# Optimization experiments

Hardware: AMD Instinct MI355X
Metric: run time of the kernel (lower is better)

The kernel has to match this reference:

```python
import jax, jax.numpy as jnp
import numpy as np
import math

B, S, H, NH = 8, 512, 1024, 16
DH = H // NH
MAX_REL = 64
LN_EPS = 1e-12


def _relpos_table(length, depth, max_rel=MAX_REL):
    # sinusoidal table over relative-distance vocab, gathered into [L, L, depth]
    vocab = 2 * max_rel + 1
    pos = np.arange(vocab, dtype=np.float32)[:, None]
    div = np.exp(np.arange(0, depth, 2, dtype=np.float32) * (-math.log(10000.0) / depth))
    table = np.zeros((vocab, depth), dtype=np.float32)
    table[:, 0::2] = np.sin(pos * div)
    table[:, 1::2] = np.cos(pos * div)
    r = np.arange(length)
    dist = np.clip(r[None, :] - r[:, None], -max_rel, max_rel) + max_rel  # [L,L], entry (i,j)=j-i
    return jnp.asarray(table[dist])  # [L, L, depth]


def _linear(x, W, b):  # torch layout: W [out, in]
    return jnp.einsum('...i,oi->...o', x, W) + b


def _gather_shift(seq, shift, valid_len):
    # seq [B,S,H]; out[i, j] = seq[i, j+shift[i]] for j < valid_len[i], else 0
    pos = jnp.arange(S)
    idx = jnp.clip(pos[None, :] + shift[:, None], 0, S - 1)  # [B,S]
    g = jnp.take_along_axis(seq, idx[:, :, None], axis=1)
    mask = pos[None, :] < valid_len[:, None]
    return jnp.where(mask[:, :, None], g, jnp.zeros((), seq.dtype))


def _nezha_attention(hs, enc, R, Wq, bq, Wk, bk, Wv, bv):
    def heads(x):  # [B,S,H] -> [B,NH,S,DH]
        return x.reshape(B, S, NH, DH).transpose(0, 2, 1, 3)
    q = heads(_linear(hs, Wq, bq))
    k = heads(_linear(enc, Wk, bk))
    v = heads(_linear(enc, Wv, bv))
    scores = jnp.einsum('bhqd,bhkd->bhqk', q, k)
    scores = scores + jnp.einsum('bhqd,qkd->bhqk', q, R)  # relative-key bias
    scores = scores / math.sqrt(DH)
    probs = jax.nn.softmax(scores, axis=-1)  # dropout: eval mode (identity)
    ctx = jnp.einsum('bhqk,bhkd->bhqd', probs, v)
    ctx = ctx + jnp.einsum('bhqk,qkd->bhqd', probs, R)  # relative-value term
    return ctx.transpose(0, 2, 1, 3).reshape(B, S, H)


def setup_inputs() -> dict:
    key = jax.random.key(0)
    ks = jax.random.split(key, 16)
    w = lambda k, shp: jax.random.normal(k, shp, jnp.float32) * 0.02
    return {
        'sequence_output': jax.random.normal(ks[0], (B, S, H), jnp.float32),
        'doc_len': jax.random.randint(ks[1], (B,), 0, 300, jnp.int32),
        'ques_len': jax.random.randint(ks[2], (B,), 0, 100, jnp.int32),
        'option_len': jax.random.randint(ks[3], (B,), 0, 100, jnp.int32),
        'Wq': w(ks[4], (H, H)), 'bq': jnp.zeros((H,), jnp.float32),
        'Wk': w(ks[5], (H, H)), 'bk': jnp.zeros((H,), jnp.float32),
        'Wv': w(ks[6], (H, H)), 'bv': jnp.zeros((H,), jnp.float32),
        'Wp': w(ks[7], (H, H)), 'bp': jnp.zeros((H,), jnp.float32),
        'Wo': w(ks[8], (H, H)), 'bo': jnp.zeros((H,), jnp.float32),
        'ln_g': jnp.ones((H,), jnp.float32), 'ln_b': jnp.zeros((H,), jnp.float32),
    }


def reference(sequence_output, doc_len, ques_len, option_len,
              Wq, bq, Wk, bk, Wv, bv, Wp, bp, Wo, bo, ln_g, ln_b):
    one = jnp.ones_like(doc_len)
    # seperate_seq (only the two tensors DUMA consumes)
    doc_seq = _gather_shift(sequence_output, one, doc_len)
    ques_opt = _gather_shift(sequence_output, doc_len + 1, ques_len + option_len)

    R = _relpos_table(S, DH)
    doc_enc = _nezha_attention(doc_seq, ques_opt, R, Wq, bq, Wk, bk, Wv, bv)
    qo_enc = _nezha_attention(ques_opt, doc_seq, R, Wq, bq, Wk, bk, Wv, bv)

    pooler = lambda x: jnp.tanh(_linear(x, Wp, bp))
    doc_pooled = pooler(doc_enc)
    qo_pooled = pooler(qo_enc)

    # BertSelfOutput: dense + (dropout=eval) + LayerNorm(residual)
    y = _linear(doc_pooled, Wo, bo) + qo_pooled
    mu = jnp.mean(y, axis=-1, keepdims=True)
    var = jnp.mean(jnp.square(y - mu), axis=-1, keepdims=True)
    y = (y - mu) * jax.lax.rsqrt(var + LN_EPS) * ln_g + ln_b

    return pooler(y)
```

## Files before the change

### kernel.cpp

```cpp
#include <hip/hip_runtime.h>
#include <hip/hip_bf16.h>
#include <cstdint>
#include <cstddef>

using bf16 = __hip_bfloat16;
typedef __attribute__((ext_vector_type(8))) short short8;
typedef __attribute__((ext_vector_type(4))) short short4v;
typedef __attribute__((ext_vector_type(4))) float f32x4;

#define KQLD 2048
#define SCL   0.18033688f
#define EXP2F(x) __builtin_amdgcn_exp2f(x)

__device__ __forceinline__ void gl2lds16(const bf16* g, void* l) {
  __builtin_amdgcn_global_load_lds((const __attribute__((address_space(1))) void*)g,
                                   (__attribute__((address_space(3))) void*)l, 16, 0, 0);
}

template<int ACT, bool OUTBF, bool HASB, int VTM>
__global__ __launch_bounds__(512)
void gemm_big(const bf16* __restrict__ A, const bf16* __restrict__ Bm,
              void* __restrict__ Cv, const float* __restrict__ bias,
              int N, int K, int lda, int ldb, int ldc, bf16* __restrict__ Vt,
              const int* __restrict__ dl, const int* __restrict__ ql,
              const int* __restrict__ ol)
{
  __shared__ __align__(16) short lA[3 * 4096];
  __shared__ __align__(16) short lB[3 * 8192];
  const int tid = threadIdx.x;
  int bx = blockIdx.x, by = blockIdx.y;
  {
    const int nwg = gridDim.x * gridDim.y;
    if ((nwg & 7) == 0) {
      int n = by * gridDim.x + bx;
      n = (n & 7) * (nwg >> 3) + (n >> 3);
      bx = n / gridDim.y;
      by = n % gridDim.y;
    }
  }
  const int m0 = bx * 128;
  const int n0 = by * 256;
  const int w = tid >> 6, lane = tid & 63;
  const int wr = (w >> 2) * 64, wc = (w & 3) * 64;
  const int lr = lane & 15, lg = lane >> 4;
  f32x4 acc[4][4] = {};

  bool live = true;
  if (VTM) {
    const int half = m0 >> 12, bb = (m0 >> 9) & 7, j0 = m0 & 511;
    const int vlen = (half == 0) ? dl[bb] : (ql[bb] + ol[bb]);
    live = (j0 < vlen);
  }

  if (live) {
    const int ra = tid >> 2;
    const int xc = ((tid & 3) ^ ((tid >> 2) & 3)) * 8;
    const int e1 = tid + 512;
    const int rb1 = e1 >> 2;
    const bf16* pa0 = A + (long)(m0 + ra) * lda + xc;
    const bf16* pb0 = Bm + (long)(n0 + ra) * ldb + xc;
    const bf16* pb1 = Bm + (long)(n0 + rb1) * ldb + xc;

    #define GSTG(k0_, ofa_, ofb_) do {                  \
      gl2lds16(pa0 + (k0_), &lA[(ofa_) + tid * 8]);     \
      gl2lds16(pb0 + (k0_), &lB[(ofb_) + tid * 8]);     \
      gl2lds16(pb1 + (k0_), &lB[(ofb_) + e1 * 8]);      \
    } while (0)

    const int nT = K >> 5;
    GSTG(0, 0, 0);
    if (nT > 1) GSTG(32, 4096, 8192);
    if (nT > 2) asm volatile("s_waitcnt vmcnt(3)" ::: "memory");
    else        asm volatile("s_waitcnt vmcnt(0)" ::: "memory");
    __builtin_amdgcn_s_barrier();
    __builtin_amdgcn_sched_barrier(0);

    const int lgx = (lg ^ (lr & 3)) * 8;
    int oa = 0, oa1 = 4096, oa2 = 8192;
    int ob = 0, ob1 = 8192, ob2 = 16384;
    for (int t = 0; t < nT; ++t) {
      if (t + 2 < nT) GSTG((t + 2) * 32, oa2, ob2);
      short8 af[4], bfr[4];
      #pragma unroll
      for (int i = 0; i < 4; ++i) {
        af[i]  = *(const short8*)(&lA[oa + (wr + i * 16 + lr) * 32 + lgx]);
        bfr[i] = *(const short8*)(&lB[ob + (wc + i * 16 + lr) * 32 + lgx]);
      }
      #pragma unroll
      for (int mf = 0; mf < 4; ++mf)
        #pragma unroll
        for (int nf = 0; nf < 4; ++nf)
          acc[mf][nf] = __builtin_amdgcn_mfma_f32_16x16x32_bf16(af[mf], bfr[nf], acc[mf][nf], 0, 0, 0);
      if (t + 1 < nT) {
        if (t + 2 < nT) asm volatile("s_waitcnt vmcnt(3)" ::: "memory");
        else            asm volatile("s_waitcnt vmcnt(0)" ::: "memory");
        __builtin_amdgcn_s_barrier();
        __builtin_amdgcn_sched_barrier(0);
        int tmp = oa; oa = oa1; oa1 = oa2; oa2 = tmp;
        tmp = ob; ob = ob1; ob1 = ob2; ob2 = tmp;
      }
    }
    #undef GSTG
  }

  #pragma unroll
  for (int nf = 0; nf < 4; ++nf) {
    const int col = n0 + wc + nf * 16 + lr;
    if (col >= N) continue;
    const float bv = HASB ? bias[col] : 0.0f;
    if (VTM && col >= 2048) {
      const int hd = col - 2048;
      const int d = hd & 63, hh = hd >> 6;
      #pragma unroll
      for (int mf = 0; mf < 4; ++mf) {
        const int row0 = m0 + wr + mf * 16 + lg * 4;
        const int zz = ((1 - (row0 >> 12)) << 7) | (((row0 >> 9) & 7) << 4) | hh;
        short4v pk;
        #pragma unroll
        for (int j = 0; j < 4; ++j)
          pk[j] = (short)__builtin_bit_cast(unsigned short,
                    __float2bfloat16(acc[mf][nf][j] + bv));
        *(short4v*)(Vt + ((long)(zz * 64 + d)) * 512 + (row0 & 511)) = pk;
      }
    } else {
      #pragma unroll
      for (int mf = 0; mf < 4; ++mf) {
        #pragma unroll
        for (int j = 0; j < 4; ++j) {
          const int row = m0 + wr + mf * 16 + lg * 4 + j;
          float x = acc[mf][nf][j] + bv;
          if (ACT == 1) x = tanhf(x);
          const long off = (long)row * ldc + col;
          if (OUTBF) ((bf16*)Cv)[off] = __float2bfloat16(x);
          else       ((float*)Cv)[off] = x;
        }
      }
    }
  }
}

template<int ACT, bool OUTBF>
__global__ __launch_bounds__(256)
void gemm_64(const bf16* __restrict__ A, const bf16* __restrict__ Bm,
             void* __restrict__ Cv, const float* __restrict__ bias,
             int K, int lda, int ldb, int ldc)
{
  __shared__ __align__(16) short lA[3 * 2048];
  __shared__ __align__(16) short lB[3 * 4096];
  const int tid = threadIdx.x;
  int bx = blockIdx.x, by = blockIdx.y;
  {
    const int nwg = gridDim.x * gridDim.y;
    if ((nwg & 7) == 0) {
      int n = by * gridDim.x + bx;
      n = (n & 7) * (nwg >> 3) + (n >> 3);
      bx = n / gridDim.y;
      by = n % gridDim.y;
    }
  }
  const int m0 = bx * 64;
  const int n0 = by * 128;
  const int w = tid >> 6, lane = tid & 63;
  const int wc = w * 32;
  const int lr = lane & 15, lg = lane >> 4;
  f32x4 acc[4][2] = {};
  const int rA = tid >> 2, cA = (tid & 3) * 8;
  const bf16* pa  = A + (long)(m0 + rA) * lda + cA;
  const bf16* pb0 = Bm + (long)(n0 + rA) * ldb + cA;
  const bf16* pb1 = Bm + (long)(n0 + 64 + rA) * ldb + cA;

  #define GS64(k0_, oa_, ob_) do {                     \
    gl2lds16(pa  + (k0_), &lA[(oa_) + tid * 8]);       \
    gl2lds16(pb0 + (k0_), &lB[(ob_) + tid * 8]);       \
    gl2lds16(pb1 + (k0_), &lB[(ob_) + 2048 + tid * 8]);\
  } while (0)

  const int nT = K >> 5;
  GS64(0, 0, 0);
  if (nT > 1) GS64(32, 2048, 4096);
  if (nT > 2) asm volatile("s_waitcnt vmcnt(3)" ::: "memory");
  else        asm volatile("s_waitcnt vmcnt(0)" ::: "memory");
  __builtin_amdgcn_s_barrier();
  __builtin_amdgcn_sched_barrier(0);

  int oa = 0, oa1 = 2048, oa2 = 4096;
  int ob = 0, ob1 = 4096, ob2 = 8192;
  for (int t = 0; t < nT; ++t) {
    if (t + 2 < nT) GS64((t + 2) * 32, oa2, ob2);
    short8 af[4], bfr[2];
    #pragma unroll
    for (int i = 0; i < 4; ++i)
      af[i] = *(const short8*)(&lA[oa + (i * 16 + lr) * 32 + lg * 8]);
    #pragma unroll
    for (int j = 0; j < 2; ++j)
      bfr[j] = *(const short8*)(&lB[ob + (wc + j * 16 + lr) * 32 + lg * 8]);
    #pragma unroll
    for (int mf = 0; mf < 4; ++mf)
      #pragma unroll
      for (int nf = 0; nf < 2; ++nf)
        acc[mf][nf] = __builtin_amdgcn_mfma_f32_16x16x32_bf16(af[mf], bfr[nf], acc[mf][nf], 0, 0, 0);
    if (t + 1 < nT) {
      if (t + 2 < nT) asm volatile("s_waitcnt vmcnt(3)" ::: "memory");
      else            asm volatile("s_waitcnt vmcnt(0)" ::: "memory");
      __builtin_amdgcn_s_barrier();
      __builtin_amdgcn_sched_barrier(0);
      int tmp = oa; oa = oa1; oa1 = oa2; oa2 = tmp;
      tmp = ob; ob = ob1; ob1 = ob2; ob2 = tmp;
    }
  }
  #undef GS64

  #pragma unroll
  for (int nf = 0; nf < 2; ++nf) {
    const int col = n0 + wc + nf * 16 + lr;
    const float bv = bias[col];
    #pragma unroll
    for (int mf = 0; mf < 4; ++mf) {
      #pragma unroll
      for (int j = 0; j < 4; ++j) {
        const int row = m0 + mf * 16 + lg * 4 + j;
        float x = acc[mf][nf][j] + bv;
        if (ACT == 1) x = tanhf(x);
        const long off = (long)row * ldc + col;
        if (OUTBF) ((bf16*)Cv)[off] = __float2bfloat16(x);
        else       ((float*)Cv)[off] = x;
      }
    }
  }
}

__global__ __launch_bounds__(256)
void k_prep(const float* __restrict__ w0, const float* __restrict__ w1,
            const float* __restrict__ w2, const float* __restrict__ w3,
            const float* __restrict__ w4, bf16* __restrict__ wdst,
            const float* __restrict__ seq, const int* __restrict__ dl,
            const int* __restrict__ ql, const int* __restrict__ ol,
            bf16* __restrict__ X, bf16* __restrict__ tbl, bf16* __restrict__ tbt,
            const float* __restrict__ bq, const float* __restrict__ bk,
            const float* __restrict__ bv, float* __restrict__ biasq)
{
  const int bid = blockIdx.x, tid = threadIdx.x;
  if (bid < 5120) {
    const int bsel = bid >> 10;
    const float* s = bsel == 0 ? w0 : bsel == 1 ? w1 : bsel == 2 ? w2 : bsel == 3 ? w3 : w4;
    const float sc = (bsel == 0) ? SCL : 1.0f;
    const long loc = ((long)(bid & 1023) * 256 + tid) * 4;
    float4 v = *(const float4*)(s + loc);
    short4v pk;
    pk[0] = (short)__builtin_bit_cast(unsigned short, __float2bfloat16(v.x * sc));
    pk[1] = (short)__builtin_bit_cast(unsigned short, __float2bfloat16(v.y * sc));
    pk[2] = (short)__builtin_bit_cast(unsigned short, __float2bfloat16(v.z * sc));
    pk[3] = (short)__builtin_bit_cast(unsigned short, __float2bfloat16(v.w * sc));
    *(short4v*)(wdst + (long)bsel * 1048576 + loc) = pk;
  } else if (bid < 13312) {
    const int row = bid - 5120;
    const int c = tid * 4;
    const int b = (row >> 9) & 7, j = row & 511;
    int vlen, src;
    if (row < 4096) { vlen = dl[b]; src = (j + 1 > 511) ? 511 : j + 1; }
    else {
      vlen = ql[b] + ol[b];
      int s2 = j + dl[b] + 1;
      src = s2 > 511 ? 511 : (s2 < 0 ? 0 : s2);
    }
    float4 v = make_float4(0, 0, 0, 0);
    if (j < vlen) v = *(const float4*)(seq + ((long)b * 512 + src) * 1024 + c);
    short4v pk;
    pk[0] = (short)__builtin_bit_cast(unsigned short, __float2bfloat16(v.x));
    pk[1] = (short)__builtin_bit_cast(unsigned short, __float2bfloat16(v.y));
    pk[2] = (short)__builtin_bit_cast(unsigned short, __float2bfloat16(v.z));
    pk[3] = (short)__builtin_bit_cast(unsigned short, __float2bfloat16(v.w));
    *(short4v*)(X + (long)row * 1024 + c) = pk;
  } else {
    for (int idx = tid; idx < 144 * 64; idx += 256) {
      const int r = idx >> 6, d = idx & 63;
      float v = 0.0f;
      if (r < 129) {
        const float dv = powf(10000.0f, -(float)(d >> 1) / 32.0f);
        const float a = (float)r * dv;
        v = (d & 1) ? cosf(a) : sinf(a);
      }
      tbl[idx] = __float2bfloat16(v);
    }
    for (int idx = tid; idx < 64 * 160; idx += 256) {
      const int d = idx / 160, rr = idx % 160;
      float v = 0.0f;
      if (rr < 129) {
        const float dv = powf(10000.0f, -(float)(d >> 1) / 32.0f);
        const float a = (float)rr * dv;
        v = (d & 1) ? cosf(a) : sinf(a);
      }
      tbt[idx] = __float2bfloat16(v);
    }
    for (int idx = tid; idx < 3072; idx += 256) {
      float v = (idx < 1024) ? bq[idx] * SCL : (idx < 2048) ? bk[idx - 1024] : bv[idx - 2048];
      biasq[idx] = v;
    }
  }
}

__global__ __launch_bounds__(1024, 4)
void k_attn(const bf16* __restrict__ QKV, const bf16* __restrict__ Vt,
            const bf16* __restrict__ tbl, const bf16* __restrict__ tbt,
            bf16* __restrict__ ctx)
{
  __shared__ __align__(16) unsigned short s_kv[16384];
  __shared__ __align__(16) unsigned short s_ptile[16][16 * 72];
  __shared__ __align__(16) unsigned short s_m[16][16 * 132];

  const int tid = threadIdx.x;
  const int wv = tid >> 6, lane = tid & 63;
  const int lr = lane & 15, lg = lane >> 4;
  const int bid = blockIdx.x;
  const int xcd = bid & 7;
  const int idx = bid >> 3;
  const int z = (xcd << 5) | (idx >> 1);
  const int g = idx & 1;
  const int attn = z >> 7, b = (z >> 4) & 7, h = z & 15;
  const int qtok0 = attn * 4096 + b * 512;
  const int ktok0 = (1 - attn) * 4096 + b * 512;
  const int q0 = g * 256 + wv * 16;
  const int q = q0 + lr;

  unsigned short* ptile = s_ptile[wv];
  unsigned short* mrow  = s_m[wv];

  const bf16* Kbase = QKV + (long)ktok0 * KQLD + 1024 + h * 64;
  const bf16* Vbase = Vt + (long)z * (64 * 512);

  const int sl = tid & 511;
  const int rs = sl >> 3, cs = (sl & 7) * 8;
  const int scz = cs ^ ((rs & 7) << 3);
  const bool isV = tid >= 512;

  short8 qf[2];
  #pragma unroll
  for (int hh = 0; hh < 2; ++hh)
    qf[hh] = *(const short8*)(QKV + (long)(qtok0 + q0 + lr) * KQLD + h * 64 + hh * 32 + lg * 8);

  #define STAGE(kvb_, koff_, voff_) do {                                            \
    if (!isV) gl2lds16(Kbase + (long)((kvb_) + rs) * KQLD + scz, &s_kv[(koff_) + sl * 8]); \
    else      gl2lds16(Vbase + (long)rs * 512 + (kvb_) + scz,    &s_kv[(voff_) + sl * 8]); \
  } while (0)

  STAGE(0, 0, 8192);

  #pragma unroll
  for (int rt = 0; rt < 9; ++rt) {
    f32x4 qa = {};
    #pragma unroll
    for (int hh = 0; hh < 2; ++hh) {
      short8 ta = *(const short8*)(tbl + (rt * 16 + lr) * 64 + hh * 32 + lg * 8);
      qa = __builtin_amdgcn_mfma_f32_16x16x32_bf16(ta, qf[hh], qa, 0, 0, 0);
    }
    if (rt < 8 || lg == 0) {
      short4v pk;
      #pragma unroll
      for (int j = 0; j < 4; ++j)
        pk[j] = (short)__builtin_bit_cast(unsigned short, __float2bfloat16(qa[j]));
      *(short4v*)(&mrow[lr * 132 + rt * 16 + lg * 4]) = pk;
    }
  }

  const int hx = (lr >> 2) & 1;
  const int lgx8 = (lg ^ (lr & 3)) * 8;
  const int lrx64 = lr * 64;

  const float bias_lo = __bfloat162float(((const bf16*)mrow)[lr * 132 + 0]);
  const float bias_hi = __bfloat162float(((const bf16*)mrow)[lr * 132 + 128]);

  float l_run = 0.f, b0 = 0.f, b1 = 0.f;
  f32x4 cacc[4] = {};

  __syncthreads();

  #pragma unroll 2
  for (int t = 0; t < 8; ++t) {
    const int kvb = t * 64;
    const int koff = (t & 1) * 4096;
    const int voff = 8192 + koff;
    if (t < 7) { const int nk = ((t + 1) & 1) * 4096; STAGE(kvb + 64, nk, 8192 + nk); }

    f32x4 sc[4] = {};
    __builtin_amdgcn_s_setprio(1);
    #pragma unroll
    for (int hh = 0; hh < 2; ++hh) {
      const int cb = ((hh ^ hx) << 5) + lgx8;
      #pragma unroll
      for (int kb4 = 0; kb4 < 4; ++kb4) {
        short8 ak = *(const short8*)(&s_kv[koff + kb4 * 1024 + lrx64 + cb]);
        sc[kb4] = __builtin_amdgcn_mfma_f32_16x16x32_bf16(ak, qf[hh], sc[kb4], 0, 0, 0);
      }
    }
    __builtin_amdgcn_s_setprio(0);

    const int cls = (kvb + 63 <= q0 - 64) ? 0 : ((kvb >= q0 + 79) ? 2 : 1);

    float pacc[4];
    if (cls == 1) {
      const bool eLo = (kvb <= q0 - 49);
      const bool eHi = (kvb + 63 >= q0 + 64);
      short4v pks[4];
      #pragma unroll
      for (int kb4 = 0; kb4 < 4; ++kb4) {
        short4v pk;
        float ps = 0.f;
        #pragma unroll
        for (int j = 0; j < 4; ++j) {
          int rel = kvb + kb4 * 16 + 4 * lg + j - q;
          int rc = rel < -64 ? -64 : (rel > 64 ? 64 : rel);
          float bias = __bfloat162float(((const bf16*)mrow)[lr * 132 + rc + 64]);
          float p = EXP2F(sc[kb4][j] + bias);
          ps += p;
          if (eLo && rel <= -64) b0 += p;
          if (eHi && rel >= 64)  b1 += p;
          pk[j] = (short)__builtin_bit_cast(unsigned short, __float2bfloat16(p));
        }
        pks[kb4] = pk;
        pacc[kb4] = ps;
        *(short4v*)(&ptile[lr * 72 + kb4 * 16 + 4 * lg]) = pk;
      }
      l_run += (pacc[0] + pacc[1]) + (pacc[2] + pacc[3]);
      #pragma unroll
      for (int kb4 = 0; kb4 < 4; ++kb4)
        #pragma unroll
        for (int j = 0; j < 4; ++j) {
          int rel = kvb + kb4 * 16 + 4 * lg + j - q;
          if (rel > -64 && rel < 64)
            mrow[lr * 132 + rel + 63] = (unsigned short)pks[kb4][j];
        }
    } else {
      const float bc = (cls == 0) ? bias_lo : bias_hi;
      #pragma unroll
      for (int kb4 = 0; kb4 < 4; ++kb4) {
        short4v pk;
        float ps = 0.f;
        #pragma unroll
        for (int j = 0; j < 4; ++j) {
          float p = EXP2F(sc[kb4][j] + bc);
          ps += p;
          pk[j] = (short)__builtin_bit_cast(unsigned short, __float2bfloat16(p));
        }
        pacc[kb4] = ps;
        *(short4v*)(&ptile[lr * 72 + kb4 * 16 + 4 * lg]) = pk;
      }
      const float ts = (pacc[0] + pacc[1]) + (pacc[2] + pacc[3]);
      l_run += ts;
      if (cls == 0) b0 += ts; else b1 += ts;
    }

    __builtin_amdgcn_s_setprio(1);
    #pragma unroll
    for (int c2 = 0; c2 < 2; ++c2) {
      short8 pa = *(const short8*)(&ptile[lr * 72 + c2 * 32 + lg * 8]);
      const int cb = ((c2 ^ hx) << 5) + lgx8;
      #pragma unroll
      for (int nf = 0; nf < 4; ++nf) {
        short8 vb = *(const short8*)(&s_kv[voff + nf * 1024 + lrx64 + cb]);
        cacc[nf] = __builtin_amdgcn_mfma_f32_16x16x32_bf16(pa, vb, cacc[nf], 0, 0, 0);
      }
    }
    __builtin_amdgcn_s_setprio(0);
    __syncthreads();
  }
  #undef STAGE

  l_run += __shfl_xor(l_run, 16); l_run += __shfl_xor(l_run, 32);
  b0 += __shfl_xor(b0, 16); b0 += __shfl_xor(b0, 32);
  b1 += __shfl_xor(b1, 16); b1 += __shfl_xor(b1, 32);
  const float inv = 1.0f / l_run;

  #pragma unroll
  for (int j = 0; j < 4; ++j) {
    float iq = __shfl(inv, 4 * lg + j);
    #pragma unroll
    for (int nf = 0; nf < 4; ++nf) cacc[nf][j] *= iq;
  }
  short8 paf[5];
  #pragma unroll
  for (int c = 0; c < 5; ++c)
    #pragma unroll
    for (int j = 0; j < 8; ++j) {
      int r = c * 32 + 8 * lg + j;
      float v = 0.f;
      if (r == 0) v = b0;
      else if (r == 128) v = b1;
      else if (r < 128) {
        int k = q + r - 64;
        if (k >= 0 && k < 512)
          v = __bfloat162float(((const bf16*)mrow)[lr * 132 + r - 1]);
      }
      bf16 vb = __float2bfloat16(v * inv);
      paf[c][j] = (short)__builtin_bit_cast(unsigned short, vb);
    }
  __builtin_amdgcn_s_setprio(1);
  #pragma unroll
  for (int c = 0; c < 5; ++c)
    #pragma unroll
    for (int nf = 0; nf < 4; ++nf) {
      short8 tb = *(const short8*)(tbt + (nf * 16 + lr) * 160 + c * 32 + lg * 8);
      cacc[nf] = __builtin_amdgcn_mfma_f32_16x16x32_bf16(paf[c], tb, cacc[nf], 0, 0, 0);
    }
  __builtin_amdgcn_s_setprio(0);
  #pragma unroll
  for (int nf = 0; nf < 4; ++nf)
    #pragma unroll
    for (int j = 0; j < 4; ++j) {
      int qq = q0 + 4 * lg + j;
      ctx[(long)(qtok0 + qq) * 1024 + h * 64 + nf * 16 + lr] = __float2bfloat16(cacc[nf][j]);
    }
}

__global__ __launch_bounds__(256) void k_ln(const float* __restrict__ y,
    const bf16* __restrict__ pooled, const float* __restrict__ g,
    const float* __restrict__ be, bf16* __restrict__ o)
{
  const int row = blockIdx.x, tid = threadIdx.x;
  float x[4], s1 = 0.0f, s2 = 0.0f;
  #pragma unroll
  for (int i = 0; i < 4; ++i) {
    const int c = tid + i * 256;
    x[i] = y[(long)row * 1024 + c] + __bfloat162float(pooled[(long)(4096 + row) * 1024 + c]);
    s1 += x[i]; s2 += x[i] * x[i];
  }
  #pragma unroll
  for (int off = 1; off < 64; off <<= 1) { s1 += __shfl_xor(s1, off); s2 += __shfl_xor(s2, off); }
  __shared__ float r1[4], r2[4];
  if ((tid & 63) == 0) { r1[tid >> 6] = s1; r2[tid >> 6] = s2; }
  __syncthreads();
  s1 = r1[0] + r1[1] + r1[2] + r1[3];
  s2 = r2[0] + r2[1] + r2[2] + r2[3];
  const float mu = s1 * (1.0f / 1024.0f);
  const float var = s2 * (1.0f / 1024.0f) - mu * mu;
  const float rs = rsqrtf(var + 1e-12f);
  #pragma unroll
  for (int i = 0; i < 4; ++i) {
    const int c = tid + i * 256;
    o[(long)row * 1024 + c] = __float2bfloat16((x[i] - mu) * rs * g[c] + be[c]);
  }
}

__global__ void k_sent(float* o, float v) { o[0] = v; }

extern "C" void kernel_launch(void* const* d_in, const int* in_sizes, int n_in,
                              void* d_out, int out_size, void* d_ws, size_t ws_size,
                              hipStream_t stream)
{
  (void)in_sizes; (void)n_in; (void)out_size;
  const float* seq = (const float*)d_in[0];
  const int*  dl = (const int*)d_in[1];
  const int*  ql = (const int*)d_in[2];
  const int*  ol = (const int*)d_in[3];
  const float* Wq = (const float*)d_in[4];  const float* bq = (const float*)d_in[5];
  const float* Wk = (const float*)d_in[6];  const float* bk = (const float*)d_in[7];
  const float* Wv = (const float*)d_in[8];  const float* bv = (const float*)d_in[9];
  const float* Wp = (const float*)d_in[10]; const float* bp = (const float*)d_in[11];
  const float* Wo = (const float*)d_in[12]; const float* bo = (const float*)d_in[13];
  const float* lng = (const float*)d_in[14]; const float* lnb = (const float*)d_in[15];
  float* out = (float*)d_out;
  char* ws = (char*)d_ws;

  size_t cur = 0;
  auto alloc = [&](size_t bts) { size_t o = cur; cur += (bts + 255) & ~(size_t)255; return o; };
  const size_t oBIAS = alloc(3072 * sizeof(float));
  const size_t oTBL  = alloc(144 * 64 * 2);
  const size_t oTBT  = alloc(64 * 160 * 2);
  const size_t oWBF  = alloc(5ull * 1048576 * 2);
  const size_t oXBF  = alloc(8192ull * 1024 * 2);
  const size_t oQKV  = alloc(8192ull * KQLD * 2);
  const size_t oQR   = alloc(8192ull * 2176 * 2);
  const size_t oBP   = alloc(256ull * 64 * 512 * 2);
  if (ws_size < cur) {
    k_sent<<<1, 1, 0, stream>>>(out, 1.0e6f + (float)(ws_size >> 20));
    return;
  }

  float* biasq = (float*)(ws + oBIAS);
  bf16* tbl = (bf16*)(ws + oTBL);
  bf16* tbt = (bf16*)(ws + oTBT);
  bf16* wqb = (bf16*)(ws + oWBF);
  bf16* wpb = wqb + 3 * 1048576;
  bf16* wob = wqb + 4 * 1048576;
  bf16* xbf = (bf16*)(ws + oXBF);
  bf16* qkv = (bf16*)(ws + oQKV);
  bf16* bpb = (bf16*)(ws + oBP);
  bf16* ctx = xbf;
  bf16* pooled = (bf16*)(ws + oQR);
  float* ybuf = (float*)(ws + oQR + 8192ull * 1024 * 2);
  bf16* yln = (bf16*)(ws + oBP);

  dim3 blk(256);
  k_prep<<<13313, blk, 0, stream>>>(Wq, Wk, Wv, Wp, Wo, wqb,
                                    seq, dl, ql, ol, xbf, tbl, tbt,
                                    bq, bk, bv, biasq);

  gemm_big<0, true, true, 1><<<dim3(64, 12, 1), dim3(512), 0, stream>>>(xbf, wqb, qkv, biasq, 3072, 1024, 1024, 1024, KQLD, bpb, dl, ql, ol);
  k_attn<<<512, dim3(1024), 0, stream>>>(qkv, bpb, tbl, tbt, ctx);

  gemm_64<1, true><<<dim3(128, 8, 1), blk, 0, stream>>>(ctx, wpb, pooled, bp, 1024, 1024, 1024, 1024);
  gemm_64<0, false><<<dim3(64, 8, 1), blk, 0, stream>>>(pooled, wob, ybuf, bo, 1024, 1024, 1024, 1024);
  k_ln<<<4096, blk, 0, stream>>>(ybuf, pooled, lng, lnb, yln);
  gemm_64<1, false><<<dim3(64, 8, 1), blk, 0, stream>>>(yln, wpb, out, bp, 1024, 1024, 1024, 1024);
}
```

Baseline: 236.7 us.

## Skip zero-padded key tiles in attention using analytic padded-key score

Attention now computes how many 64-key tiles hold valid (non-padded) keys from the sequence lengths, and runs the MMA loop only over those tiles. For padded keys, whose K and V rows are just the projection biases, it computes one shared score from a single padded K row and adds the softmax mass and bias-V contribution analytically, still applying the relative-position bias per key. This removes QK and PV matrix work and K/V staging for padded tiles. In exchange the loop is no longer unrolled, extra per-row bookkeeping is added, and correctness relies on padded rows being exactly bias-only, which holds by construction of the gather.

```diff
diff --git a/kernel.cpp b/kernel.cpp
--- a/kernel.cpp
+++ b/kernel.cpp
@@ -302,6 +302,8 @@
 __global__ __launch_bounds__(1024, 4)
 void k_attn(const bf16* __restrict__ QKV, const bf16* __restrict__ Vt,
             const bf16* __restrict__ tbl, const bf16* __restrict__ tbt,
+            const float* __restrict__ biasq, const int* __restrict__ dl,
+            const int* __restrict__ ql, const int* __restrict__ ol,
             bf16* __restrict__ ctx)
 {
   __shared__ __align__(16) unsigned short s_kv[16384];
@@ -322,6 +324,11 @@
   const int q0 = g * 256 + wv * 16;
   const int q = q0 + lr;
 
+  const int vk = (attn == 0) ? (ql[b] + ol[b]) : dl[b];
+  int nLive = (vk + 63) >> 6;
+  if (nLive < 1) nLive = 1;
+  if (nLive > 8) nLive = 8;
+
   unsigned short* ptile = s_ptile[wv];
   unsigned short* mrow  = s_m[wv];
 
@@ -333,10 +340,12 @@
   const int scz = cs ^ ((rs & 7) << 3);
   const bool isV = tid >= 512;
 
-  short8 qf[2];
-  #pragma unroll
-  for (int hh = 0; hh < 2; ++hh)
+  short8 qf[2], kp[2];
+  #pragma unroll
+  for (int hh = 0; hh < 2; ++hh) {
     qf[hh] = *(const short8*)(QKV + (long)(qtok0 + q0 + lr) * KQLD + h * 64 + hh * 32 + lg * 8);
+    kp[hh] = *(const short8*)(Kbase + (long)511 * KQLD + hh * 32 + lg * 8);
+  }
 
   #define STAGE(kvb_, koff_, voff_) do {                                            \
     if (!isV) gl2lds16(Kbase + (long)((kvb_) + rs) * KQLD + scz, &s_kv[(koff_) + sl * 8]); \
@@ -362,6 +371,16 @@
     }
   }
 
+  float sp = 0.f;
+  #pragma unroll
+  for (int hh = 0; hh < 2; ++hh)
+    #pragma unroll
+    for (int j = 0; j < 8; ++j)
+      sp += __bfloat162float(__builtin_bit_cast(bf16, (unsigned short)qf[hh][j])) *
+            __bfloat162float(__builtin_bit_cast(bf16, (unsigned short)kp[hh][j]));
+  sp += __shfl_xor(sp, 16); sp += __shfl_xor(sp, 32);
+  const float s_pad = sp;
+
   const int hx = (lr >> 2) & 1;
   const int lgx8 = (lg ^ (lr & 3)) * 8;
   const int lrx64 = lr * 64;
@@ -369,17 +388,16 @@
   const float bias_lo = __bfloat162float(((const bf16*)mrow)[lr * 132 + 0]);
   const float bias_hi = __bfloat162float(((const bf16*)mrow)[lr * 132 + 128]);
 
-  float l_run = 0.f, b0 = 0.f, b1 = 0.f;
+  float l_run = 0.f, b0 = 0.f, b1 = 0.f, pad_ps = 0.f;
   f32x4 cacc[4] = {};
 
   __syncthreads();
 
-  #pragma unroll 2
-  for (int t = 0; t < 8; ++t) {
+  for (int t = 0; t < nLive; ++t) {
     const int kvb = t * 64;
     const int koff = (t & 1) * 4096;
     const int voff = 8192 + koff;
-    if (t < 7) { const int nk = ((t + 1) & 1) * 4096; STAGE(kvb + 64, nk, 8192 + nk); }
+    if (t + 1 < nLive) { const int nk = ((t + 1) & 1) * 4096; STAGE(kvb + 64, nk, 8192 + nk); }
 
     f32x4 sc[4] = {};
     __builtin_amdgcn_s_setprio(1);
@@ -465,16 +483,70 @@
   }
   #undef STAGE
 
+  for (int t = nLive; t < 8; ++t) {
+    const int kvb = t * 64;
+    const int cls = (kvb + 63 <= q0 - 64) ? 0 : ((kvb >= q0 + 79) ? 2 : 1);
+    if (cls == 1) {
+      const bool eLo = (kvb <= q0 - 49);
+      const bool eHi = (kvb + 63 >= q0 + 64);
+      short4v pks[4];
+      float pacc[4];
+      #pragma unroll
+      for (int kb4 = 0; kb4 < 4; ++kb4) {
+        short4v pk;
+        float ps = 0.f;
+        #pragma unroll
+        for (int j = 0; j < 4; ++j) {
+          int rel = kvb + kb4 * 16 + 4 * lg + j - q;
+          int rc = rel < -64 ? -64 : (rel > 64 ? 64 : rel);
+          float bias = __bfloat162float(((const bf16*)mrow)[lr * 132 + rc + 64]);
+          float p = EXP2F(s_pad + bias);
+          ps += p;
+          if (eLo && rel <= -64) b0 += p;
+          if (eHi && rel >= 64)  b1 += p;
+          bf16 pb = __float2bfloat16(p);
+          pad_ps += __bfloat162float(pb);
+          pk[j] = (short)__builtin_bit_cast(unsigned short, pb);
+        }
+        pks[kb4] = pk;
+        pacc[kb4] = ps;
+      }
+      l_run += (pacc[0] + pacc[1]) + (pacc[2] + pacc[3]);
+      #pragma unroll
+      for (int kb4 = 0; kb4 < 4; ++kb4)
+        #pragma unroll
+        for (int j = 0; j < 4; ++j) {
+          int rel = kvb + kb4 * 16 + 4 * lg + j - q;
+          if (rel > -64 && rel < 64)
+            mrow[lr * 132 + rel + 63] = (unsigned short)pks[kb4][j];
+        }
+    } else {
+      const float bc = (cls == 0) ? bias_lo : bias_hi;
+      const float p = EXP2F(s_pad + bc);
+      const float ts = 16.0f * p;
+      l_run += ts;
+      if (cls == 0) b0 += ts; else b1 += ts;
+      pad_ps += 16.0f * __bfloat162float(__float2bfloat16(p));
+    }
+  }
+
   l_run += __shfl_xor(l_run, 16); l_run += __shfl_xor(l_run, 32);
   b0 += __shfl_xor(b0, 16); b0 += __shfl_xor(b0, 32);
   b1 += __shfl_xor(b1, 16); b1 += __shfl_xor(b1, 32);
+  pad_ps += __shfl_xor(pad_ps, 16); pad_ps += __shfl_xor(pad_ps, 32);
   const float inv = 1.0f / l_run;
 
+  float vv[4];
+  #pragma unroll
+  for (int nf = 0; nf < 4; ++nf)
+    vv[nf] = __bfloat162float(__float2bfloat16(biasq[2048 + h * 64 + nf * 16 + lr]));
   #pragma unroll
   for (int j = 0; j < 4; ++j) {
     float iq = __shfl(inv, 4 * lg + j);
-    #pragma unroll
-    for (int nf = 0; nf < 4; ++nf) cacc[nf][j] *= iq;
+    float pq = __shfl(pad_ps, 4 * lg + j);
+    #pragma unroll
+    for (int nf = 0; nf < 4; ++nf)
+      cacc[nf][j] = (cacc[nf][j] + pq * vv[nf]) * iq;
   }
   short8 paf[5];
   #pragma unroll
@@ -595,7 +667,7 @@
                                     bq, bk, bv, biasq);
 
   gemm_big<0, true, true, 1><<<dim3(64, 12, 1), dim3(512), 0, stream>>>(xbf, wqb, qkv, biasq, 3072, 1024, 1024, 1024, KQLD, bpb, dl, ql, ol);
-  k_attn<<<512, dim3(1024), 0, stream>>>(qkv, bpb, tbl, tbt, ctx);
+  k_attn<<<512, dim3(1024), 0, stream>>>(qkv, bpb, tbl, tbt, biasq, dl, ql, ol, ctx);
 
   gemm_64<1, true><<<dim3(128, 8, 1), blk, 0, stream>>>(ctx, wpb, pooled, bp, 1024, 1024, 1024, 1024);
   gemm_64<0, false><<<dim3(64, 8, 1), blk, 0, stream>>>(pooled, wob, ybuf, bo, 1024, 1024, 1024, 1024);
```

Result: faster. 227.8 us (-3.7%).
